# Optimization experiments

Measured on AMD Instinct MI355X. Metric: run time of the kernel, lower is better.

The kernel has to match this reference:

```python
import jax, jax.numpy as jnp
import numpy as np

B, N, D, H = 2, 2048, 768, 12
HD = D // H  # head_dim = 64
SCALE = HD ** -0.5


def setup_inputs() -> dict:
    key = jax.random.key(0)
    ks = jax.random.split(key, 8)
    return {
        "x": jax.random.normal(ks[0], (B, N, D), jnp.float32),
        "masks": jax.random.uniform(ks[1], (B, H, N), jnp.float32),
        "lambda_r": jax.random.uniform(ks[2], (B, H), jnp.float32) * 4.0 + 1.0,
        "theta_r": jax.random.uniform(ks[3], (B, H), jnp.float32),
        "mask_weights": jax.random.uniform(ks[4], (B, H), jnp.float32),
        "qkv_w": jax.random.normal(ks[5], (D, 3 * D), jnp.float32) * (D ** -0.5),
        "qkv_b": jnp.zeros((3 * D,), jnp.float32),
        "proj_w": jax.random.normal(ks[6], (D, D), jnp.float32) * (D ** -0.5),
        "proj_b": jnp.zeros((D,), jnp.float32),
    }


def reference(x, masks, lambda_r, theta_r, mask_weights, qkv_w, qkv_b, proj_w, proj_b):
    # qkv projection: [B,N,3D] -> [3,B,H,N,HD]
    qkv = (x @ qkv_w + qkv_b).reshape(B, N, 3, H, HD).transpose(2, 0, 3, 1, 4)
    q, k, v = qkv[0], qkv[1], qkv[2]
    # raw scores [B,H,N,N]
    attn = jnp.einsum('bhqd,bhkd->bhqk', q, k) * SCALE
    # region gate: sigmoid(lambda * (m_i*m_j - theta)) multiplied into scores pre-softmax
    gate = jax.nn.sigmoid(
        lambda_r[:, :, None, None]
        * (masks[:, :, :, None] * masks[:, :, None, :] - theta_r[:, :, None, None])
    )
    attn = jax.nn.softmax(attn * gate, axis=-1)  # dropout is identity in eval
    out = jnp.einsum('bhqk,bhkd->bqhd', attn, v).reshape(B, N, D)
    # per-head output scaling via mask_weights
    out = out * jnp.repeat(mask_weights, HD, axis=-1)[:, None, :]
    return out @ proj_w + proj_b
```

## Files before the change

### kernel.cpp

```cpp
#include <hip/hip_runtime.h>

typedef unsigned short u16;
typedef unsigned int u32;
typedef __attribute__((ext_vector_type(8))) short short8;
typedef __attribute__((ext_vector_type(4))) float f32x4;

#define NB 2
#define NSEQ 2048
#define DIM 768
#define NH 12
#define HDIM 64

#define LOG2E 1.44269504088896f
#define CFOLD 0.18033688f

#if defined(__has_builtin)
#if __has_builtin(__builtin_amdgcn_exp2f)
#define EXPB(x) __builtin_amdgcn_exp2f(x)
#else
#define EXPB(x) exp2f(x)
#endif
#if __has_builtin(__builtin_amdgcn_rcpf)
#define RCP(x) __builtin_amdgcn_rcpf(x)
#else
#define RCP(x) (1.0f / (x))
#endif
#else
#define EXPB(x) exp2f(x)
#define RCP(x) (1.0f / (x))
#endif

__device__ __forceinline__ u16 f2bf(float x) {
    union { float f; unsigned u; } v; v.f = x;
    unsigned r = v.u + 0x7fffu + ((v.u >> 16) & 1u);
    return (u16)(r >> 16);
}

__device__ __forceinline__ u32 pack_bf16(float a, float b) {
    union { float f; u32 u; } A, B; A.f = a; B.f = b;
    u32 ra = A.u + 0x7fffu + ((A.u >> 16) & 1u);
    u32 rb = B.u + 0x7fffu + ((B.u >> 16) & 1u);
    return __builtin_amdgcn_perm(rb, ra, 0x07060302u);
}

__device__ __forceinline__ f32x4 mfma16(short8 a, short8 b, f32x4 c) {
    return __builtin_amdgcn_mfma_f32_16x16x32_bf16(a, b, c, 0, 0, 0);
}

__device__ __forceinline__ void glds16(const u16* g, u16* l) {
    __builtin_amdgcn_global_load_lds((const __attribute__((address_space(1))) u32*)g,
                                     (__attribute__((address_space(3))) u32*)l, 16, 0, 0);
}

__global__ __launch_bounds__(256) void prep(const float* __restrict__ x, u16* __restrict__ xb,
                                            const float* __restrict__ qkv_w, u16* __restrict__ wq,
                                            const float* __restrict__ proj_w, u16* __restrict__ wp) {
    const int t = threadIdx.x;
    int bid = blockIdx.x;
    if (bid < 3072) {
        int i = (bid * 256 + t) * 4;
        float4 v = *(const float4*)(x + i);
        *(uint2*)(xb + i) = make_uint2(pack_bf16(v.x, v.y), pack_bf16(v.z, v.w));
        return;
    }
    const float* in; u16* outp; int rows, cols, bx, by;
    if (bid < 3072 + 1728) {
        bid -= 3072; in = qkv_w; outp = wq; rows = 768; cols = 2304;
        bx = bid % 72; by = bid / 72;
    } else {
        bid -= 4800; in = proj_w; outp = wp; rows = 768; cols = 768;
        bx = bid % 24; by = bid / 24;
    }
    __shared__ float tile[32][33];
    int c0 = bx * 32, r0 = by * 32;
    int tx = t & 31, ty = t >> 5;
    #pragma unroll
    for (int i = 0; i < 32; i += 8)
        tile[ty + i][tx] = in[(size_t)(r0 + ty + i) * cols + c0 + tx];
    __syncthreads();
    #pragma unroll
    for (int i = 0; i < 32; i += 8)
        outp[(size_t)(c0 + ty + i) * rows + r0 + tx] = f2bf(tile[tx][ty + i]);
}

__global__ __launch_bounds__(256) void vtrans(const u16* __restrict__ vin,
                                              u16* __restrict__ vout) {
    __shared__ __align__(16) u16 tile[64][72];
    const int bh = blockIdx.y;
    const int n0 = blockIdx.x * 64;
    const int t = threadIdx.x;
    const size_t base = (size_t)bh * NSEQ * HDIM;
    int r = t >> 3, cb = (t & 7) * 8;
    *(uint4*)&tile[r][cb]      = *(const uint4*)&vin[base + (size_t)(n0 + r) * HDIM + cb];
    *(uint4*)&tile[r + 32][cb] = *(const uint4*)&vin[base + (size_t)(n0 + r + 32) * HDIM + cb];
    __syncthreads();
    #pragma unroll
    for (int half = 0; half < 2; half++) {
        int d = (t >> 3) + half * 32;
        int nb = (t & 7) * 8;
        short8 v;
        #pragma unroll
        for (int j = 0; j < 8; j++) v[j] = (short)tile[nb + j][d];
        *(short8*)&vout[base + (size_t)d * NSEQ + n0 + nb] = v;
    }
}

__global__ __launch_bounds__(256) void gemm_qkv(const u16* __restrict__ A,
                                                const u16* __restrict__ BT,
                                                const float* __restrict__ bias,
                                                u16* __restrict__ qo,
                                                u16* __restrict__ ko,
                                                u16* __restrict__ vo) {
    __shared__ __align__(16) u16 As[2][4096];
    __shared__ __align__(16) u16 Bs[2][4096];
    const int bm = blockIdx.y * 128, bn = blockIdx.x * 128;
    const int t = threadIdx.x;
    const int lane = t & 63, wave = t >> 6;
    const int l15 = lane & 15, quad = lane >> 4;
    const int wm = (wave >> 1) * 64, wn = (wave & 1) * 64;

    const int srow = t >> 2;
    const int sc = (t & 3) ^ ((srow >> 1) & 3);
    const u16* ga = A + (size_t)(bm + srow) * DIM + sc * 8;
    const u16* gb = BT + (size_t)(bn + srow) * DIM + sc * 8;
    const int ldst = wave * 512;
    const int swz = (quad ^ ((l15 >> 1) & 3)) * 8;

    f32x4 acc[4][4] = {};
    glds16(ga, &As[0][ldst]); glds16(ga + (size_t)64 * DIM, &As[0][2048 + ldst]);
    glds16(gb, &Bs[0][ldst]); glds16(gb + (size_t)64 * DIM, &Bs[0][2048 + ldst]);
    ga += 32; gb += 32;

    const int NKT = DIM / 32;
    for (int kt = 0; kt < NKT; kt++) {
        const int buf = kt & 1;
        __syncthreads();
        if (kt + 1 < NKT) {
            glds16(ga, &As[buf ^ 1][ldst]); glds16(ga + (size_t)64 * DIM, &As[buf ^ 1][2048 + ldst]);
            glds16(gb, &Bs[buf ^ 1][ldst]); glds16(gb + (size_t)64 * DIM, &Bs[buf ^ 1][2048 + ldst]);
            ga += 32; gb += 32;
        }
        short8 af[4], bf[4];
        #pragma unroll
        for (int i = 0; i < 4; i++) af[i] = *(const short8*)&As[buf][(wm + i * 16 + l15) * 32 + swz];
        #pragma unroll
        for (int j = 0; j < 4; j++) bf[j] = *(const short8*)&Bs[buf][(wn + j * 16 + l15) * 32 + swz];
        #pragma unroll
        for (int i = 0; i < 4; i++)
            #pragma unroll
            for (int j = 0; j < 4; j++)
                acc[i][j] = mfma16(af[i], bf[j], acc[i][j]);
    }

    #pragma unroll
    for (int i = 0; i < 4; i++) {
        int mr = bm + wm + i * 16 + quad * 4;
        int b = mr >> 11, nn = mr & 2047;
        #pragma unroll
        for (int j = 0; j < 4; j++) {
            int ncol = bn + wn + j * 16 + l15;
            int w = ncol / DIM, rem = ncol - w * DIM;
            int h = rem >> 6, hd = rem & 63;
            u16* dst = (w == 0) ? qo : (w == 1) ? ko : vo;
            float bb = bias[ncol];
            size_t idx = (((size_t)(b * NH + h)) * NSEQ + nn) * HDIM + hd;
            #pragma unroll
            for (int r = 0; r < 4; r++)
                dst[idx + (size_t)r * HDIM] = f2bf(acc[i][j][r] + bb);
        }
    }
}

__global__ __launch_bounds__(256) void attn_kernel(const u16* __restrict__ Q,
                                                   const u16* __restrict__ Kg,
                                                   const u16* __restrict__ Vt,
                                                   const float* __restrict__ masks,
                                                   const float* __restrict__ lambda_r,
                                                   const float* __restrict__ theta_r,
                                                   const float* __restrict__ mask_w,
                                                   u16* __restrict__ AO) {
    const int bh = blockIdx.y;
    const int b = bh / NH, h = bh % NH;
    const int qb = blockIdx.x * 64;
    const int t = threadIdx.x, wave = t >> 6, lane = t & 63;
    const int l15 = lane & 15, quad = lane >> 4;

    __shared__ __align__(16) u16 Ks[2][4096];
    __shared__ __align__(16) u16 Vs[2][4096];
    __shared__ __align__(16) u16 Ps[4][1152];
    __shared__ __align__(16) float mks[2][64];

    const float lam = lambda_r[bh], th = theta_r[bh], mw = mask_w[bh];
    const float Bfac = lam * th * LOG2E;

    const size_t base = (size_t)bh * (NSEQ * HDIM);
    const int qrow = qb + wave * 16;

    const u16* Qr = Q + base + (size_t)(qrow + l15) * HDIM;
    short8 bq0 = *(const short8*)(Qr + quad * 8);
    short8 bq1 = *(const short8*)(Qr + 32 + quad * 8);
    const float Afac = -lam * LOG2E * masks[bh * NSEQ + qrow + l15];

    const int srow = t >> 3;
    const int gc = (t & 7) ^ (srow & 7);
    const u16* kgp = Kg + base + (size_t)srow * HDIM + gc * 8;
    const u16* vgp = Vt + base + (size_t)srow * NSEQ + gc * 8;
    const int ldst = wave * 512;

    const int ph = (quad ^ (l15 & 7)) * 8;
    const int kb0 = l15 * 64 + ph, kb1 = l15 * 64 + (ph ^ 32);
    u16* PsW = Ps[wave];
    const int pw = l15 * 72 + quad * 4;
    const int prd = l15 * 72 + quad * 8;
    const float* mrow = masks + bh * NSEQ;

    float lsum = 0.f;
    f32x4 O[4] = {};

    glds16(kgp, &Ks[0][ldst]);
    glds16(kgp + 32 * HDIM, &Ks[0][2048 + ldst]);
    glds16(vgp, &Vs[0][ldst]);
    glds16(vgp + (size_t)32 * NSEQ, &Vs[0][2048 + ldst]);
    if (t < 16) *(float4*)&mks[0][t * 4] = *(const float4*)&mrow[t * 4];

    const int NT = NSEQ / 64;
    for (int kt = 0; kt < NT; kt++) {
        const int buf = kt & 1;
        __syncthreads();
        if (kt + 1 < NT) {
            const u16* kn = kgp + (kt + 1) * 64 * HDIM;
            const u16* vn = vgp + (kt + 1) * 64;
            glds16(kn, &Ks[buf ^ 1][ldst]);
            glds16(kn + 32 * HDIM, &Ks[buf ^ 1][2048 + ldst]);
            glds16(vn, &Vs[buf ^ 1][ldst]);
            glds16(vn + (size_t)32 * NSEQ, &Vs[buf ^ 1][2048 + ldst]);
            if (t < 16) *(float4*)&mks[buf ^ 1][t * 4] = *(const float4*)&mrow[(kt + 1) * 64 + t * 4];
        }
        const u16* KsB = Ks[buf];
        const u16* VsB = Vs[buf];
        const float* mkb = mks[buf];

        #pragma unroll
        for (int c = 0; c < 4; c++) {
            short8 ak0 = *(const short8*)&KsB[kb0 + c * 1024];
            short8 ak1 = *(const short8*)&KsB[kb1 + c * 1024];
            f32x4 S = {0.f, 0.f, 0.f, 0.f};
            S = mfma16(ak0, bq0, S);
            S = mfma16(ak1, bq1, S);
            float4 mkv = *(const float4*)&mkb[c * 16 + quad * 4];
            float p[4];
            #pragma unroll
            for (int r = 0; r < 4; r++) {
                float mk = (r == 0) ? mkv.x : (r == 1) ? mkv.y : (r == 2) ? mkv.z : mkv.w;
                float e = EXPB(fmaf(mk, Afac, Bfac));
                float gate = RCP(1.0f + e);
                p[r] = EXPB(S[r] * CFOLD * gate);
            }
            lsum += (p[0] + p[1]) + (p[2] + p[3]);
            *(uint2*)&PsW[pw + c * 16] = make_uint2(pack_bf16(p[0], p[1]), pack_bf16(p[2], p[3]));
        }

        #pragma unroll
        for (int kc = 0; kc < 2; kc++) {
            const int vb = kc ? kb1 : kb0;
            short8 bp = *(const short8*)&PsW[prd + kc * 32];
            #pragma unroll
            for (int dt = 0; dt < 4; dt++) {
                short8 av = *(const short8*)&VsB[vb + dt * 1024];
                O[dt] = mfma16(av, bp, O[dt]);
            }
        }
    }

    lsum += __shfl_xor(lsum, 16);
    lsum += __shfl_xor(lsum, 32);
    float sc = mw / lsum;
    u16* aor = AO + ((size_t)(b * NSEQ) + qrow + l15) * DIM + h * HDIM + quad * 4;
    #pragma unroll
    for (int dt = 0; dt < 4; dt++) {
        *(uint2*)(aor + dt * 16) = make_uint2(pack_bf16(O[dt][0] * sc, O[dt][1] * sc),
                                              pack_bf16(O[dt][2] * sc, O[dt][3] * sc));
    }
}

__global__ __launch_bounds__(256) void gemm_proj(const u16* __restrict__ A,
                                                 const u16* __restrict__ BT,
                                                 const float* __restrict__ bias,
                                                 float* __restrict__ outp) {
    __shared__ __align__(16) u16 As[2][4096];
    __shared__ __align__(16) u16 Bs[2][2048];
    const int bm = blockIdx.y * 128, bn = blockIdx.x * 64;
    const int t = threadIdx.x;
    const int lane = t & 63, wave = t >> 6;
    const int l15 = lane & 15, quad = lane >> 4;
    const int wm = wave * 32;

    const int srow = t >> 2;
    const int sc = (t & 3) ^ ((srow >> 1) & 3);
    const u16* ga = A + (size_t)(bm + srow) * DIM + sc * 8;
    const u16* gb = BT + (size_t)(bn + srow) * DIM + sc * 8;
    const int ldst = wave * 512;
    const int swz = (quad ^ ((l15 >> 1) & 3)) * 8;

    f32x4 acc[2][4] = {};
    glds16(ga, &As[0][ldst]); glds16(ga + (size_t)64 * DIM, &As[0][2048 + ldst]);
    glds16(gb, &Bs[0][ldst]);
    ga += 32; gb += 32;

    const int NKT = DIM / 32;
    for (int kt = 0; kt < NKT; kt++) {
        const int buf = kt & 1;
        __syncthreads();
        if (kt + 1 < NKT) {
            glds16(ga, &As[buf ^ 1][ldst]); glds16(ga + (size_t)64 * DIM, &As[buf ^ 1][2048 + ldst]);
            glds16(gb, &Bs[buf ^ 1][ldst]);
            ga += 32; gb += 32;
        }
        short8 af[2], bf[4];
        #pragma unroll
        for (int i = 0; i < 2; i++) af[i] = *(const short8*)&As[buf][(wm + i * 16 + l15) * 32 + swz];
        #pragma unroll
        for (int j = 0; j < 4; j++) bf[j] = *(const short8*)&Bs[buf][(j * 16 + l15) * 32 + swz];
        #pragma unroll
        for (int i = 0; i < 2; i++)
            #pragma unroll
            for (int j = 0; j < 4; j++)
                acc[i][j] = mfma16(af[i], bf[j], acc[i][j]);
    }

    #pragma unroll
    for (int i = 0; i < 2; i++) {
        int mr = bm + wm + i * 16 + quad * 4;
        #pragma unroll
        for (int j = 0; j < 4; j++) {
            int ncol = bn + j * 16 + l15;
            float bb = bias[ncol];
            #pragma unroll
            for (int r = 0; r < 4; r++)
                outp[(size_t)(mr + r) * DIM + ncol] = acc[i][j][r] + bb;
        }
    }
}

extern "C" void kernel_launch(void* const* d_in, const int* in_sizes, int n_in,
                              void* d_out, int out_size, void* d_ws, size_t ws_size,
                              hipStream_t stream) {
    const float* x            = (const float*)d_in[0];
    const float* masks        = (const float*)d_in[1];
    const float* lambda_r     = (const float*)d_in[2];
    const float* theta_r      = (const float*)d_in[3];
    const float* mask_weights = (const float*)d_in[4];
    const float* qkv_w        = (const float*)d_in[5];
    const float* qkv_b        = (const float*)d_in[6];
    const float* proj_w       = (const float*)d_in[7];
    const float* proj_b       = (const float*)d_in[8];
    float* outp = (float*)d_out;

    const size_t SZH = (size_t)NB * NH * NSEQ * HDIM;
    u16* xb    = (u16*)d_ws;
    u16* wqkvT = xb + (size_t)4096 * 768;
    u16* wprT  = wqkvT + (size_t)2304 * 768;
    u16* qg    = wprT + (size_t)768 * 768;
    u16* kg    = qg + SZH;
    u16* vtmp  = kg + SZH;
    u16* vt    = vtmp + SZH;
    u16* ao    = xb;

    prep<<<dim3(3072 + 1728 + 576), 256, 0, stream>>>(x, xb, qkv_w, wqkvT, proj_w, wprT);
    gemm_qkv<<<dim3(2304 / 128, 4096 / 128), 256, 0, stream>>>(xb, wqkvT, qkv_b, qg, kg, vtmp);
    vtrans<<<dim3(NSEQ / 64, NB * NH), 256, 0, stream>>>(vtmp, vt);
    attn_kernel<<<dim3(NSEQ / 64, NB * NH), 256, 0, stream>>>(qg, kg, vt, masks, lambda_r,
                                                              theta_r, mask_weights, ao);
    gemm_proj<<<dim3(768 / 64, 4096 / 128), 256, 0, stream>>>(ao, wprT, proj_b, outp);
}
```

Baseline: 202.2 us.

## Fuse V transpose into QKV GEMM epilogue and hoist gate computation

After: 192.4 us. 4.8% less time.

```diff
diff --git a/kernel.cpp b/kernel.cpp
--- a/kernel.cpp
+++ b/kernel.cpp
@@ -43,6 +43,11 @@
     return __builtin_amdgcn_perm(rb, ra, 0x07060302u);
 }
 
+__device__ __forceinline__ u32 pack_rtn(float a, float b) {
+    union { float f; u32 u; } A, B; A.f = a; B.f = b;
+    return __builtin_amdgcn_perm(B.u + 0x8000u, A.u + 0x8000u, 0x07060302u);
+}
+
 __device__ __forceinline__ f32x4 mfma16(short8 a, short8 b, f32x4 c) {
     return __builtin_amdgcn_mfma_f32_16x16x32_bf16(a, b, c, 0, 0, 0);
 }
@@ -83,36 +88,13 @@
         outp[(size_t)(c0 + ty + i) * rows + r0 + tx] = f2bf(tile[tx][ty + i]);
 }
 
-__global__ __launch_bounds__(256) void vtrans(const u16* __restrict__ vin,
-                                              u16* __restrict__ vout) {
-    __shared__ __align__(16) u16 tile[64][72];
-    const int bh = blockIdx.y;
-    const int n0 = blockIdx.x * 64;
-    const int t = threadIdx.x;
-    const size_t base = (size_t)bh * NSEQ * HDIM;
-    int r = t >> 3, cb = (t & 7) * 8;
-    *(uint4*)&tile[r][cb]      = *(const uint4*)&vin[base + (size_t)(n0 + r) * HDIM + cb];
-    *(uint4*)&tile[r + 32][cb] = *(const uint4*)&vin[base + (size_t)(n0 + r + 32) * HDIM + cb];
-    __syncthreads();
-    #pragma unroll
-    for (int half = 0; half < 2; half++) {
-        int d = (t >> 3) + half * 32;
-        int nb = (t & 7) * 8;
-        short8 v;
-        #pragma unroll
-        for (int j = 0; j < 8; j++) v[j] = (short)tile[nb + j][d];
-        *(short8*)&vout[base + (size_t)d * NSEQ + n0 + nb] = v;
-    }
-}
-
 __global__ __launch_bounds__(256) void gemm_qkv(const u16* __restrict__ A,
                                                 const u16* __restrict__ BT,
                                                 const float* __restrict__ bias,
                                                 u16* __restrict__ qo,
                                                 u16* __restrict__ ko,
                                                 u16* __restrict__ vo) {
-    __shared__ __align__(16) u16 As[2][4096];
-    __shared__ __align__(16) u16 Bs[2][4096];
+    __shared__ __align__(16) u16 pool[17408];
     const int bm = blockIdx.y * 128, bn = blockIdx.x * 128;
     const int t = threadIdx.x;
     const int lane = t & 63, wave = t >> 6;
@@ -125,26 +107,29 @@
     const u16* gb = BT + (size_t)(bn + srow) * DIM + sc * 8;
     const int ldst = wave * 512;
     const int swz = (quad ^ ((l15 >> 1) & 3)) * 8;
+    u16* As0 = pool;
+    u16* Bs0 = pool + 8192;
 
     f32x4 acc[4][4] = {};
-    glds16(ga, &As[0][ldst]); glds16(ga + (size_t)64 * DIM, &As[0][2048 + ldst]);
-    glds16(gb, &Bs[0][ldst]); glds16(gb + (size_t)64 * DIM, &Bs[0][2048 + ldst]);
+    glds16(ga, As0 + ldst); glds16(ga + (size_t)64 * DIM, As0 + 2048 + ldst);
+    glds16(gb, Bs0 + ldst); glds16(gb + (size_t)64 * DIM, Bs0 + 2048 + ldst);
     ga += 32; gb += 32;
 
     const int NKT = DIM / 32;
     for (int kt = 0; kt < NKT; kt++) {
-        const int buf = kt & 1;
+        const int bo = (kt & 1) * 4096;
         __syncthreads();
         if (kt + 1 < NKT) {
-            glds16(ga, &As[buf ^ 1][ldst]); glds16(ga + (size_t)64 * DIM, &As[buf ^ 1][2048 + ldst]);
-            glds16(gb, &Bs[buf ^ 1][ldst]); glds16(gb + (size_t)64 * DIM, &Bs[buf ^ 1][2048 + ldst]);
+            const int bn2 = (bo ^ 4096);
+            glds16(ga, As0 + bn2 + ldst); glds16(ga + (size_t)64 * DIM, As0 + bn2 + 2048 + ldst);
+            glds16(gb, Bs0 + bn2 + ldst); glds16(gb + (size_t)64 * DIM, Bs0 + bn2 + 2048 + ldst);
             ga += 32; gb += 32;
         }
         short8 af[4], bf[4];
         #pragma unroll
-        for (int i = 0; i < 4; i++) af[i] = *(const short8*)&As[buf][(wm + i * 16 + l15) * 32 + swz];
-        #pragma unroll
-        for (int j = 0; j < 4; j++) bf[j] = *(const short8*)&Bs[buf][(wn + j * 16 + l15) * 32 + swz];
+        for (int i = 0; i < 4; i++) af[i] = *(const short8*)&As0[bo + (wm + i * 16 + l15) * 32 + swz];
+        #pragma unroll
+        for (int j = 0; j < 4; j++) bf[j] = *(const short8*)&Bs0[bo + (wn + j * 16 + l15) * 32 + swz];
         #pragma unroll
         for (int i = 0; i < 4; i++)
             #pragma unroll
@@ -152,21 +137,45 @@
                 acc[i][j] = mfma16(af[i], bf[j], acc[i][j]);
     }
 
+    __syncthreads();
+    u16* Cs = pool;
     #pragma unroll
     for (int i = 0; i < 4; i++) {
-        int mr = bm + wm + i * 16 + quad * 4;
-        int b = mr >> 11, nn = mr & 2047;
+        int row0 = wm + i * 16 + quad * 4;
         #pragma unroll
         for (int j = 0; j < 4; j++) {
-            int ncol = bn + wn + j * 16 + l15;
-            int w = ncol / DIM, rem = ncol - w * DIM;
-            int h = rem >> 6, hd = rem & 63;
-            u16* dst = (w == 0) ? qo : (w == 1) ? ko : vo;
-            float bb = bias[ncol];
-            size_t idx = (((size_t)(b * NH + h)) * NSEQ + nn) * HDIM + hd;
+            int lcol = wn + j * 16 + l15;
+            float bb = bias[bn + lcol];
             #pragma unroll
             for (int r = 0; r < 4; r++)
-                dst[idx + (size_t)r * HDIM] = f2bf(acc[i][j][r] + bb);
+                Cs[(row0 + r) * 136 + lcol] = f2bf(acc[i][j][r] + bb);
+        }
+    }
+    __syncthreads();
+
+    const int w = bn / DIM;
+    const int h0 = (bn - w * DIM) >> 6;
+    const int b = bm >> 11, nnb = bm & 2047;
+    if (w < 2) {
+        u16* dst = w ? ko : qo;
+        #pragma unroll
+        for (int p = 0; p < 8; p++) {
+            int row = p * 16 + (t >> 4);
+            int chunk = t & 15;
+            short8 v = *(const short8*)&Cs[row * 136 + chunk * 8];
+            *(short8*)&dst[(((size_t)(b * NH + h0 + (chunk >> 3))) * NSEQ + nnb + row) * HDIM +
+                           (chunk & 7) * 8] = v;
+        }
+    } else {
+        #pragma unroll
+        for (int p = 0; p < 8; p++) {
+            int hdf = p * 16 + (t >> 4);
+            int nn0 = (t & 15) * 8;
+            short8 v;
+            #pragma unroll
+            for (int k = 0; k < 8; k++) v[k] = (short)Cs[(nn0 + k) * 136 + hdf];
+            *(short8*)&vo[(((size_t)(b * NH + h0 + (hdf >> 6))) * HDIM + (hdf & 63)) * NSEQ +
+                          nnb + nn0] = v;
         }
     }
 }
@@ -240,6 +249,18 @@
         const u16* VsB = Vs[buf];
         const float* mkb = mks[buf];
 
+        float gp[4][4];
+        #pragma unroll
+        for (int c = 0; c < 4; c++) {
+            float4 mkv = *(const float4*)&mkb[c * 16 + quad * 4];
+            #pragma unroll
+            for (int r = 0; r < 4; r++) {
+                float mk = (r == 0) ? mkv.x : (r == 1) ? mkv.y : (r == 2) ? mkv.z : mkv.w;
+                float e = EXPB(fmaf(mk, Afac, Bfac));
+                gp[c][r] = CFOLD * RCP(1.0f + e);
+            }
+        }
+
         #pragma unroll
         for (int c = 0; c < 4; c++) {
             short8 ak0 = *(const short8*)&KsB[kb0 + c * 1024];
@@ -247,17 +268,11 @@
             f32x4 S = {0.f, 0.f, 0.f, 0.f};
             S = mfma16(ak0, bq0, S);
             S = mfma16(ak1, bq1, S);
-            float4 mkv = *(const float4*)&mkb[c * 16 + quad * 4];
             float p[4];
             #pragma unroll
-            for (int r = 0; r < 4; r++) {
-                float mk = (r == 0) ? mkv.x : (r == 1) ? mkv.y : (r == 2) ? mkv.z : mkv.w;
-                float e = EXPB(fmaf(mk, Afac, Bfac));
-                float gate = RCP(1.0f + e);
-                p[r] = EXPB(S[r] * CFOLD * gate);
-            }
+            for (int r = 0; r < 4; r++) p[r] = EXPB(S[r] * gp[c][r]);
             lsum += (p[0] + p[1]) + (p[2] + p[3]);
-            *(uint2*)&PsW[pw + c * 16] = make_uint2(pack_bf16(p[0], p[1]), pack_bf16(p[2], p[3]));
+            *(uint2*)&PsW[pw + c * 16] = make_uint2(pack_rtn(p[0], p[1]), pack_rtn(p[2], p[3]));
         }
 
         #pragma unroll
@@ -278,8 +293,8 @@
     u16* aor = AO + ((size_t)(b * NSEQ) + qrow + l15) * DIM + h * HDIM + quad * 4;
     #pragma unroll
     for (int dt = 0; dt < 4; dt++) {
-        *(uint2*)(aor + dt * 16) = make_uint2(pack_bf16(O[dt][0] * sc, O[dt][1] * sc),
-                                              pack_bf16(O[dt][2] * sc, O[dt][3] * sc));
+        *(uint2*)(aor + dt * 16) = make_uint2(pack_rtn(O[dt][0] * sc, O[dt][1] * sc),
+                                              pack_rtn(O[dt][2] * sc, O[dt][3] * sc));
     }
 }
 
@@ -362,13 +377,11 @@
     u16* wprT  = wqkvT + (size_t)2304 * 768;
     u16* qg    = wprT + (size_t)768 * 768;
     u16* kg    = qg + SZH;
-    u16* vtmp  = kg + SZH;
-    u16* vt    = vtmp + SZH;
+    u16* vt    = kg + SZH;
     u16* ao    = xb;
 
     prep<<<dim3(3072 + 1728 + 576), 256, 0, stream>>>(x, xb, qkv_w, wqkvT, proj_w, wprT);
-    gemm_qkv<<<dim3(2304 / 128, 4096 / 128), 256, 0, stream>>>(xb, wqkvT, qkv_b, qg, kg, vtmp);
-    vtrans<<<dim3(NSEQ / 64, NB * NH), 256, 0, stream>>>(vtmp, vt);
+    gemm_qkv<<<dim3(2304 / 128, 4096 / 128), 256, 0, stream>>>(xb, wqkvT, qkv_b, qg, kg, vt);
     attn_kernel<<<dim3(NSEQ / 64, NB * NH), 256, 0, stream>>>(qg, kg, vt, masks, lambda_r,
                                                               theta_r, mask_weights, ao);
     gemm_proj<<<dim3(768 / 64, 4096 / 128), 256, 0, stream>>>(ao, wprT, proj_b, outp);
```
